# Performance work log

Hardware: AMD Instinct MI355X
Metric: run time of the kernel (lower is better)

## Reference

```python
import jax, jax.numpy as jnp
import numpy as np
import math

B, S, D = 16, 2048, 128

def setup_inputs() -> dict:
    key = jax.random.key(0)
    k1, k2, k3, k4 = jax.random.split(key, 4)
    query = jax.random.normal(k1, (B, S, D), dtype=jnp.float32)
    key_t = jax.random.normal(k2, (B, S, D), dtype=jnp.float32)
    value = jax.random.normal(k3, (B, S, D), dtype=jnp.float32)
    attn_mask = jax.random.randint(k4, (B, S, S), 0, 2).astype(bool)
    return {"query": query, "key": key_t, "value": value, "attn_mask": attn_mask}

def reference(query, key, value, attn_mask):
    # score = Q K^T / sqrt(d)  -> [B, Sq, Sk]
    scale = 1.0 / math.sqrt(query.shape[-1])
    score = jnp.einsum('bqd,bkd->bqk', query, key) * scale
    # faithful quirk: masked positions are replaced by the VALUE 1e-9 (not -inf)
    mask_score = jnp.where(attn_mask, jnp.float32(1e-9), score)
    # faithful quirk: softmax over dim=1 (the query axis), as in the torch source
    score_matrix = jax.nn.softmax(mask_score, axis=1)
    # output = softmax(scores) @ V  -> [B, Sq, D]
    output = jnp.einsum('bqk,bkd->bqd', score_matrix, value)
    return output
```

## Files before the change

kernel.cpp:

```cpp
#include <hip/hip_runtime.h>
#include <math.h>

#define NB 16
#define SS 2048
#define DQ 128
#define SCALE 0.08838834764831845f

typedef __bf16 bf16x8 __attribute__((ext_vector_type(8)));
typedef unsigned short ushort8_t __attribute__((ext_vector_type(8)));
typedef float floatx4 __attribute__((ext_vector_type(4)));

__device__ __forceinline__ unsigned short f2bf(float x) {
  unsigned int u = __float_as_uint(x);
  u += 0x7fffu + ((u >> 16) & 1u);
  return (unsigned short)(u >> 16);
}
union FragU { ushort8_t u; bf16x8 b; };
__device__ __forceinline__ bf16x8 ld_frag(const unsigned short* p) {
  FragU t; t.u = *(const ushort8_t*)p; return t.b;
}
__device__ __forceinline__ floatx4 mfma16(bf16x8 a, bf16x8 b, floatx4 c) {
  return __builtin_amdgcn_mfma_f32_16x16x32_bf16(a, b, c, 0, 0, 0);
}


__global__ void zero_accum(float* __restrict__ O) {
  float* p = O + (size_t)blockIdx.x * SS * DQ + 16 * DQ;
#pragma unroll
  for (int i = 0; i < 8; ++i) p[threadIdx.x + 256 * i] = 0.f;
}

__global__ __launch_bounds__(256, 3) void pass1_colsum(
    const float* __restrict__ Q, const float* __restrict__ K,
    const int* __restrict__ M, float* __restrict__ O)
{
  const int k0  = blockIdx.x * 64;
  const int b   = blockIdx.y;
  const int qc  = blockIdx.z;
  const int tid = threadIdx.x;
  const int w = tid >> 6, lane = tid & 63, l15 = lane & 15, quad = lane >> 4;

  __shared__ unsigned short Kbf[64][136];
  __shared__ unsigned short Qbf[128][136];
  __shared__ float red[4][64];

  const float* Qb = Q + (size_t)b * SS * DQ;
  const float* Kb = K + (size_t)b * SS * DQ;
  const int*   Mb = M + (size_t)b * SS * SS;

#pragma unroll
  for (int r = 0; r < 8; ++r) {
    int idx = tid + r * 256;
    int row = idx >> 5, c4 = (idx & 31) * 4;
    float4 v = *(const float4*)(Kb + (size_t)(k0 + row) * DQ + c4);
    *(ushort4*)&Kbf[row][c4] = make_ushort4(f2bf(v.x), f2bf(v.y), f2bf(v.z), f2bf(v.w));
  }

  float colacc[16];
#pragma unroll
  for (int t = 0; t < 16; ++t) colacc[t] = 0.f;

  for (int qi = 0; qi < 4; ++qi) {
    const int q0 = qc * 512 + qi * 128;
    int4 mv[4][2];
#pragma unroll
    for (int i = 0; i < 4; ++i)
#pragma unroll
      for (int j = 0; j < 2; ++j)
        mv[i][j] = *(const int4*)(Mb + (size_t)(q0 + 32 * w + 16 * j + l15) * SS
                                  + k0 + 16 * i + quad * 4);
    __syncthreads();
#pragma unroll
    for (int r = 0; r < 16; ++r) {
      int idx = tid + r * 256;
      int row = idx >> 5, c4 = (idx & 31) * 4;
      float4 v = *(const float4*)(Qb + (size_t)(q0 + row) * DQ + c4);
      *(ushort4*)&Qbf[row][c4] = make_ushort4(f2bf(v.x), f2bf(v.y), f2bf(v.z), f2bf(v.w));
    }
    __syncthreads();

    floatx4 acc[4][2];
#pragma unroll
    for (int i = 0; i < 4; ++i)
#pragma unroll
      for (int j = 0; j < 2; ++j) acc[i][j] = (floatx4){0.f, 0.f, 0.f, 0.f};

#pragma unroll
    for (int d0 = 0; d0 < DQ; d0 += 32) {
      bf16x8 a[4], bb[2];
#pragma unroll
      for (int i = 0; i < 4; ++i) a[i] = ld_frag(&Kbf[16 * i + l15][d0 + quad * 8]);
#pragma unroll
      for (int j = 0; j < 2; ++j) bb[j] = ld_frag(&Qbf[32 * w + 16 * j + l15][d0 + quad * 8]);
#pragma unroll
      for (int i = 0; i < 4; ++i)
#pragma unroll
        for (int j = 0; j < 2; ++j)
          acc[i][j] = mfma16(a[i], bb[j], acc[i][j]);
    }
#pragma unroll
    for (int i = 0; i < 4; ++i)
#pragma unroll
      for (int j = 0; j < 2; ++j) {
        int mm[4] = {mv[i][j].x, mv[i][j].y, mv[i][j].z, mv[i][j].w};
#pragma unroll
        for (int r = 0; r < 4; ++r) {
          float s = mm[r] ? 1e-9f : acc[i][j][r] * SCALE;
          colacc[i * 4 + r] += __expf(s);
        }
      }
  }

#pragma unroll
  for (int t = 0; t < 16; ++t) {
    colacc[t] += __shfl_xor(colacc[t], 1, 64);
    colacc[t] += __shfl_xor(colacc[t], 2, 64);
    colacc[t] += __shfl_xor(colacc[t], 4, 64);
    colacc[t] += __shfl_xor(colacc[t], 8, 64);
  }
  if (l15 == 0) {
#pragma unroll
    for (int i = 0; i < 4; ++i)
#pragma unroll
      for (int r = 0; r < 4; ++r)
        red[w][16 * i + quad * 4 + r] = colacc[i * 4 + r];
  }
  __syncthreads();
  if (tid < 64) {
    float s = red[0][tid] + red[1][tid] + red[2][tid] + red[3][tid];
    atomicAdd(O + (size_t)b * SS * DQ + 16 * DQ + k0 + tid, s);
  }
}

__global__ void combine_linv(float* __restrict__ O) {
  const int b  = blockIdx.x;
  const int jb = blockIdx.y * 4;
  float* Ob = O + (size_t)b * SS * DQ;
#pragma unroll
  for (int it = 0; it < 8; ++it) {
    int k = threadIdx.x + 256 * it;
    float inv = 1.0f / Ob[16 * DQ + k];
#pragma unroll
    for (int j = 0; j < 4; ++j)
      Ob[(size_t)(64 * (jb + j)) * DQ + k] = inv;
  }
}

__global__ __launch_bounds__(256, 2) void pass2_out(
    const float* __restrict__ Q, const float* __restrict__ K,
    const float* __restrict__ V, const int* __restrict__ M,
    float* __restrict__ O)
{
  const int b = blockIdx.y, q0 = blockIdx.x * 64;
  const int tid = threadIdx.x;
  const int w = tid >> 6, lane = tid & 63, l15 = lane & 15, quad = lane >> 4;

  __shared__ unsigned short Qbf[64][136];
  __shared__ unsigned short Kbf[64][136];
  __shared__ unsigned short Es[64][72];
  __shared__ unsigned short Wt[128][72];
  __shared__ float Li[SS];

  const float* Qb = Q + (size_t)b * SS * DQ;
  const float* Kb = K + (size_t)b * SS * DQ;
  const float* Vb = V + (size_t)b * SS * DQ;
  const int*   Mb = M + (size_t)b * SS * SS;

  {
    const float* src = O + ((size_t)b * SS + q0) * DQ;
#pragma unroll
    for (int r = 0; r < 2; ++r) {
      int idx = (tid + r * 256) * 4;
      *(float4*)&Li[idx] = *(const float4*)(src + idx);
    }
  }
#pragma unroll
  for (int r = 0; r < 8; ++r) {
    int idx = tid + r * 256;
    int row = idx >> 5, c4 = (idx & 31) * 4;
    float4 v = *(const float4*)(Qb + (size_t)(q0 + row) * DQ + c4);
    *(ushort4*)&Qbf[row][c4] = make_ushort4(f2bf(v.x), f2bf(v.y), f2bf(v.z), f2bf(v.w));
  }
  __syncthreads();

  floatx4 accO[8];
#pragma unroll
  for (int j = 0; j < 8; ++j) accO[j] = (floatx4){0.f, 0.f, 0.f, 0.f};

  const int* mrow = Mb + (size_t)(q0 + 16 * w + l15) * SS;

  for (int k0 = 0; k0 < SS; k0 += 64) {
    int4 mv[4];
#pragma unroll
    for (int j = 0; j < 4; ++j)
      mv[j] = *(const int4*)(mrow + k0 + 16 * j + quad * 4);
    __syncthreads();

#pragma unroll
    for (int r = 0; r < 8; ++r) {
      int idx = tid + r * 256;
      int row = idx >> 5, c4 = (idx & 31) * 4;
      float4 v = *(const float4*)(Kb + (size_t)(k0 + row) * DQ + c4);
      *(ushort4*)&Kbf[row][c4] = make_ushort4(f2bf(v.x), f2bf(v.y), f2bf(v.z), f2bf(v.w));
    }
#pragma unroll
    for (int r = 0; r < 4; ++r) {
      int idx = tid + r * 256;
      int k2  = (idx >> 5) * 2;
      int c4  = (idx & 31) * 4;
      float4 va = *(const float4*)(Vb + (size_t)(k0 + k2) * DQ + c4);
      float4 vb = *(const float4*)(Vb + (size_t)(k0 + k2 + 1) * DQ + c4);
      float fa[4] = {va.x, va.y, va.z, va.w};
      float fb[4] = {vb.x, vb.y, vb.z, vb.w};
#pragma unroll
      for (int i = 0; i < 4; ++i) {
        int d  = c4 + i;
        int kk = k2 ^ ((((unsigned)d >> 2) & 7) << 3);
        *(ushort2*)&Wt[d][kk] = make_ushort2(f2bf(fa[i]), f2bf(fb[i]));
      }
    }
    __syncthreads();

    floatx4 acc[4];
#pragma unroll
    for (int j = 0; j < 4; ++j) acc[j] = (floatx4){0.f, 0.f, 0.f, 0.f};
#pragma unroll
    for (int d0 = 0; d0 < DQ; d0 += 32) {
      bf16x8 bq = ld_frag(&Qbf[16 * w + l15][d0 + quad * 8]);
#pragma unroll
      for (int j = 0; j < 4; ++j) {
        bf16x8 ak = ld_frag(&Kbf[16 * j + l15][d0 + quad * 8]);
        acc[j] = mfma16(ak, bq, acc[j]);
      }
    }
#pragma unroll
    for (int j = 0; j < 4; ++j) {
      float4 liv = *(const float4*)&Li[k0 + 16 * j + quad * 4];
      float lv[4] = {liv.x, liv.y, liv.z, liv.w};
      int mm[4] = {mv[j].x, mv[j].y, mv[j].z, mv[j].w};
      unsigned short es[4];
#pragma unroll
      for (int r = 0; r < 4; ++r) {
        float s = mm[r] ? 1e-9f : acc[j][r] * SCALE;
        es[r] = f2bf(__expf(s) * lv[r]);
      }
      *(ushort4*)&Es[16 * w + l15][16 * j + quad * 4] =
          make_ushort4(es[0], es[1], es[2], es[3]);
    }
    __syncthreads();

#pragma unroll
    for (int c = 0; c < 2; ++c) {
      bf16x8 be = ld_frag(&Es[16 * w + l15][32 * c + quad * 8]);
#pragma unroll
      for (int j = 0; j < 8; ++j) {
        int d  = 16 * j + l15;
        int kk = (32 * c + quad * 8) ^ ((((unsigned)d >> 2) & 7) << 3);
        bf16x8 aw = ld_frag(&Wt[d][kk]);
        accO[j] = mfma16(aw, be, accO[j]);
      }
    }
  }

#pragma unroll
  for (int j = 0; j < 8; ++j) {
    float* op = O + ((size_t)b * SS + q0 + 16 * w + l15) * DQ + 16 * j + quad * 4;
    *(float4*)op = make_float4(accO[j][0], accO[j][1], accO[j][2], accO[j][3]);
  }
}

extern "C" void kernel_launch(void* const* d_in, const int* in_sizes, int n_in,
                              void* d_out, int out_size, void* d_ws, size_t ws_size,
                              hipStream_t stream) {
  const float* Q = (const float*)d_in[0];
  const float* K = (const float*)d_in[1];
  const float* V = (const float*)d_in[2];
  const int*   M = (const int*)d_in[3];
  float* O = (float*)d_out;
  (void)d_ws; (void)ws_size;

  zero_accum<<<dim3(NB), 256, 0, stream>>>(O);
  pass1_colsum<<<dim3(32, NB, 4), 256, 0, stream>>>(Q, K, M, O);
  combine_linv<<<dim3(NB, 8), 256, 0, stream>>>(O);
  pass2_out<<<dim3(32, NB), 256, 0, stream>>>(Q, K, V, M, O);
}
```

Baseline: 593.8 us.

## Shrink LDS use and raise occupancy in both attention passes

Pass1 now processes 64-query tiles per iteration instead of 128, halving the Q shared buffer and the per-wave accumulator set, and raises launch bounds to 4 blocks per CU. Pass2 keeps the Q fragments in registers instead of LDS, moves the mask load later in the loop, drops one barrier before the P·V MFMAs (each wave only reads its own Es rows), and raises launch bounds to 3. The aim is more resident waves to hide memory latency, at the cost of register pressure, more iterations in pass1, and possible spills.

```diff
diff --git a/kernel.cpp b/kernel.cpp
--- a/kernel.cpp
+++ b/kernel.cpp
@@ -30,7 +30,7 @@
   for (int i = 0; i < 8; ++i) p[threadIdx.x + 256 * i] = 0.f;
 }
 
-__global__ __launch_bounds__(256, 3) void pass1_colsum(
+__global__ __launch_bounds__(256, 4) void pass1_colsum(
     const float* __restrict__ Q, const float* __restrict__ K,
     const int* __restrict__ M, float* __restrict__ O)
 {
@@ -41,7 +41,7 @@
   const int w = tid >> 6, lane = tid & 63, l15 = lane & 15, quad = lane >> 4;
 
   __shared__ unsigned short Kbf[64][136];
-  __shared__ unsigned short Qbf[128][136];
+  __shared__ unsigned short Qbf[64][136];
   __shared__ float red[4][64];
 
   const float* Qb = Q + (size_t)b * SS * DQ;
@@ -60,55 +60,45 @@
 #pragma unroll
   for (int t = 0; t < 16; ++t) colacc[t] = 0.f;
 
-  for (int qi = 0; qi < 4; ++qi) {
-    const int q0 = qc * 512 + qi * 128;
-    int4 mv[4][2];
-#pragma unroll
-    for (int i = 0; i < 4; ++i)
-#pragma unroll
-      for (int j = 0; j < 2; ++j)
-        mv[i][j] = *(const int4*)(Mb + (size_t)(q0 + 32 * w + 16 * j + l15) * SS
-                                  + k0 + 16 * i + quad * 4);
-    __syncthreads();
-#pragma unroll
-    for (int r = 0; r < 16; ++r) {
+  const int qlane = 16 * w + l15;
+
+  for (int qi = 0; qi < 8; ++qi) {
+    const int q0 = qc * 512 + qi * 64;
+    __syncthreads();
+#pragma unroll
+    for (int r = 0; r < 8; ++r) {
       int idx = tid + r * 256;
       int row = idx >> 5, c4 = (idx & 31) * 4;
       float4 v = *(const float4*)(Qb + (size_t)(q0 + row) * DQ + c4);
       *(ushort4*)&Qbf[row][c4] = make_ushort4(f2bf(v.x), f2bf(v.y), f2bf(v.z), f2bf(v.w));
     }
-    __syncthreads();
-
-    floatx4 acc[4][2];
+    int4 mv[4];
 #pragma unroll
     for (int i = 0; i < 4; ++i)
-#pragma unroll
-      for (int j = 0; j < 2; ++j) acc[i][j] = (floatx4){0.f, 0.f, 0.f, 0.f};
-
+      mv[i] = *(const int4*)(Mb + (size_t)(q0 + qlane) * SS + k0 + 16 * i + quad * 4);
+    __syncthreads();
+
+    floatx4 acc[4];
+#pragma unroll
+    for (int i = 0; i < 4; ++i) acc[i] = (floatx4){0.f, 0.f, 0.f, 0.f};
 #pragma unroll
     for (int d0 = 0; d0 < DQ; d0 += 32) {
-      bf16x8 a[4], bb[2];
-#pragma unroll
-      for (int i = 0; i < 4; ++i) a[i] = ld_frag(&Kbf[16 * i + l15][d0 + quad * 8]);
-#pragma unroll
-      for (int j = 0; j < 2; ++j) bb[j] = ld_frag(&Qbf[32 * w + 16 * j + l15][d0 + quad * 8]);
-#pragma unroll
-      for (int i = 0; i < 4; ++i)
-#pragma unroll
-        for (int j = 0; j < 2; ++j)
-          acc[i][j] = mfma16(a[i], bb[j], acc[i][j]);
-    }
-#pragma unroll
-    for (int i = 0; i < 4; ++i)
-#pragma unroll
-      for (int j = 0; j < 2; ++j) {
-        int mm[4] = {mv[i][j].x, mv[i][j].y, mv[i][j].z, mv[i][j].w};
-#pragma unroll
-        for (int r = 0; r < 4; ++r) {
-          float s = mm[r] ? 1e-9f : acc[i][j][r] * SCALE;
-          colacc[i * 4 + r] += __expf(s);
-        }
-      }
+      bf16x8 bq = ld_frag(&Qbf[qlane][d0 + quad * 8]);
+#pragma unroll
+      for (int i = 0; i < 4; ++i) {
+        bf16x8 ak = ld_frag(&Kbf[16 * i + l15][d0 + quad * 8]);
+        acc[i] = mfma16(ak, bq, acc[i]);
+      }
+    }
+#pragma unroll
+    for (int i = 0; i < 4; ++i) {
+      int mm[4] = {mv[i].x, mv[i].y, mv[i].z, mv[i].w};
+#pragma unroll
+      for (int r = 0; r < 4; ++r) {
+        float s = mm[r] ? 1e-9f : acc[i][r] * SCALE;
+        colacc[i * 4 + r] += __expf(s);
+      }
+    }
   }
 
 #pragma unroll
@@ -146,7 +136,7 @@
   }
 }
 
-__global__ __launch_bounds__(256, 2) void pass2_out(
+__global__ __launch_bounds__(256, 3) void pass2_out(
     const float* __restrict__ Q, const float* __restrict__ K,
     const float* __restrict__ V, const int* __restrict__ M,
     float* __restrict__ O)
@@ -155,7 +145,6 @@
   const int tid = threadIdx.x;
   const int w = tid >> 6, lane = tid & 63, l15 = lane & 15, quad = lane >> 4;
 
-  __shared__ unsigned short Qbf[64][136];
   __shared__ unsigned short Kbf[64][136];
   __shared__ unsigned short Es[64][72];
   __shared__ unsigned short Wt[128][72];
@@ -174,14 +163,17 @@
       *(float4*)&Li[idx] = *(const float4*)(src + idx);
     }
   }
-#pragma unroll
-  for (int r = 0; r < 8; ++r) {
-    int idx = tid + r * 256;
-    int row = idx >> 5, c4 = (idx & 31) * 4;
-    float4 v = *(const float4*)(Qb + (size_t)(q0 + row) * DQ + c4);
-    *(ushort4*)&Qbf[row][c4] = make_ushort4(f2bf(v.x), f2bf(v.y), f2bf(v.z), f2bf(v.w));
-  }
-  __syncthreads();
+  FragU qf[4];
+  {
+    const float* qrow = Qb + (size_t)(q0 + 16 * w + l15) * DQ;
+#pragma unroll
+    for (int i = 0; i < 4; ++i) {
+      float4 a = *(const float4*)(qrow + 32 * i + quad * 8);
+      float4 c = *(const float4*)(qrow + 32 * i + quad * 8 + 4);
+      qf[i].u = (ushort8_t){f2bf(a.x), f2bf(a.y), f2bf(a.z), f2bf(a.w),
+                            f2bf(c.x), f2bf(c.y), f2bf(c.z), f2bf(c.w)};
+    }
+  }
 
   floatx4 accO[8];
 #pragma unroll
@@ -190,10 +182,6 @@
   const int* mrow = Mb + (size_t)(q0 + 16 * w + l15) * SS;
 
   for (int k0 = 0; k0 < SS; k0 += 64) {
-    int4 mv[4];
-#pragma unroll
-    for (int j = 0; j < 4; ++j)
-      mv[j] = *(const int4*)(mrow + k0 + 16 * j + quad * 4);
     __syncthreads();
 
 #pragma unroll
@@ -219,17 +207,21 @@
         *(ushort2*)&Wt[d][kk] = make_ushort2(f2bf(fa[i]), f2bf(fb[i]));
       }
     }
+    int4 mv[4];
+#pragma unroll
+    for (int j = 0; j < 4; ++j)
+      mv[j] = *(const int4*)(mrow + k0 + 16 * j + quad * 4);
     __syncthreads();
 
     floatx4 acc[4];
 #pragma unroll
     for (int j = 0; j < 4; ++j) acc[j] = (floatx4){0.f, 0.f, 0.f, 0.f};
 #pragma unroll
-    for (int d0 = 0; d0 < DQ; d0 += 32) {
-      bf16x8 bq = ld_frag(&Qbf[16 * w + l15][d0 + quad * 8]);
+    for (int i = 0; i < 4; ++i) {
+      bf16x8 bq = qf[i].b;
 #pragma unroll
       for (int j = 0; j < 4; ++j) {
-        bf16x8 ak = ld_frag(&Kbf[16 * j + l15][d0 + quad * 8]);
+        bf16x8 ak = ld_frag(&Kbf[16 * j + l15][32 * i + quad * 8]);
         acc[j] = mfma16(ak, bq, acc[j]);
       }
     }
@@ -247,8 +239,6 @@
       *(ushort4*)&Es[16 * w + l15][16 * j + quad * 4] =
           make_ushort4(es[0], es[1], es[2], es[3]);
     }
-    __syncthreads();
-
 #pragma unroll
     for (int c = 0; c < 2; ++c) {
       bf16x8 be = ld_frag(&Es[16 * w + l15][32 * c + quad * 8]);
```

New measurement: 576.8 us. 1.03x faster.
